# Performance work log

Measured on AMD Instinct MI355X. Metric: run time of the kernel, lower is better.

## Reference

```python
import jax, jax.numpy as jnp
import numpy as np

DIM = 256
NUM_HEADS = 8
HEAD_DIM = DIM // NUM_HEADS


def setup_inputs() -> dict:
    key = jax.random.key(0)
    k1, k2, k3, k4 = jax.random.split(key, 4)
    b, n = 4, 2048
    x = jax.random.normal(k1, (b, n, DIM), dtype=jnp.float32)
    # Linear weights with fan-in scaling (matches nn.Linear init magnitude,
    # keeps exp(qk) numerically sane since the original has no max-subtraction).
    Wqkv = jax.random.normal(k2, (DIM, 3 * DIM), dtype=jnp.float32) * (DIM ** -0.5)
    Wout = jax.random.normal(k3, (DIM, DIM), dtype=jnp.float32) * (DIM ** -0.5)
    bout = jax.random.normal(k4, (DIM,), dtype=jnp.float32) * 0.01
    return {"x": x, "Wqkv": Wqkv, "Wout": Wout, "bout": bout}


def reference(x, Wqkv, Wout, bout):
    b, n, d = x.shape
    h, hd = NUM_HEADS, HEAD_DIM
    scale = hd ** -0.5
    qkv = x @ Wqkv  # [b, n, 3d]
    q, k, v = jnp.split(qkv, 3, axis=-1)
    # [b, h, n, hd]
    q = q.reshape(b, n, h, hd).transpose(0, 2, 1, 3) * scale
    k = k.reshape(b, n, h, hd).transpose(0, 2, 1, 3)
    v = v.reshape(b, n, h, hd).transpose(0, 2, 1, 3)
    # Original KeOps path: unnormalized exp (no max-subtraction), separate
    # numerator / denominator reductions, eps in denominator.
    scores = jnp.einsum('bhnd,bhmd->bhnm', q, k)  # [b, h, n, n]
    e = jnp.exp(scores)
    denom = jnp.sum(e, axis=-1, keepdims=True)          # [b, h, n, 1]
    numer = jnp.einsum('bhnm,bhmd->bhnd', e, v)         # [b, h, n, hd]
    out = numer / (denom + 1e-6)
    out = out.transpose(0, 2, 1, 3).reshape(b, n, d)
    return out @ Wout + bout
```

## Files before the change

### kernel.cpp

```cpp
#include <hip/hip_runtime.h>

#define DIM 256
#define NHEADS 8
#define HDIM 32

typedef _Float16 half8_t __attribute__((ext_vector_type(8)));
typedef _Float16 half4_t __attribute__((ext_vector_type(4)));
typedef float float4_t __attribute__((ext_vector_type(4)));

__device__ __forceinline__ void gload_lds16(const void* g, void* l) {
    __builtin_amdgcn_global_load_lds((const __attribute__((address_space(1))) void*)g,
                                     (__attribute__((address_space(3))) void*)l,
                                     16, 0, 0);
}

#define QSCALE 0.25503093964976485f

__global__ __launch_bounds__(256) void prep_w(const float* __restrict__ Wqkv,
                                              const float* __restrict__ Wout,
                                              _Float16* __restrict__ WqT,
                                              _Float16* __restrict__ WoT) {
    __shared__ float ts[32][33];
    const int bid = blockIdx.x, t = threadIdx.x;
    const float* src; _Float16* dst; int N, kb, nb;
    if (bid < 192) { src = Wqkv; dst = WqT; N = 768; nb = bid % 24; kb = bid / 24; }
    else           { int b3 = bid - 192; src = Wout; dst = WoT; N = 256; nb = b3 % 8; kb = b3 / 8; }
    const int tx = t & 31, ty = t >> 5;
    #pragma unroll
    for (int i = 0; i < 4; ++i)
        ts[ty + i * 8][tx] = src[(size_t)(kb * 32 + ty + i * 8) * N + nb * 32 + tx];
    __syncthreads();
    #pragma unroll
    for (int i = 0; i < 4; ++i) {
        int nl = ty + i * 8;
        dst[(size_t)(nb * 32 + nl) * 256 + kb * 32 + tx] = (_Float16)ts[tx][nl];
    }
}

__global__ __launch_bounds__(256) void gemm_qkv(const float* __restrict__ x,
                                                const _Float16* __restrict__ BT,
                                                _Float16* __restrict__ qh,
                                                _Float16* __restrict__ kpack,
                                                _Float16* __restrict__ vp) {
    __shared__ alignas(16) _Float16 As[64 * 32];
    __shared__ alignas(16) _Float16 Bs[128 * 32];
    const int t = threadIdx.x, lane = t & 63, wave = t >> 6;
    const int l16 = lane & 15, quad = lane >> 4;
    const int m0 = blockIdx.y * 64, n0 = blockIdx.x * 128;
    const int wr = (wave >> 1) * 32, wc = (wave & 1) * 64;
    const int K = 256;

    float4_t acc[2][4];
    #pragma unroll
    for (int i = 0; i < 2; ++i)
        #pragma unroll
        for (int j = 0; j < 4; ++j) acc[i][j] = (float4_t){0.f, 0.f, 0.f, 0.f};

    const int arow = t >> 2;
    const int acol = (t & 3) * 8;
    const int srow = lane >> 2;
    const int scol = (lane & 3) * 8;

    for (int k0 = 0; k0 < K; k0 += 32) {
        {
            const float* xp = x + (size_t)(m0 + arow) * K + k0 + acol;
            float tmp[8];
            *reinterpret_cast<float4*>(tmp)     = *reinterpret_cast<const float4*>(xp);
            *reinterpret_cast<float4*>(tmp + 4) = *reinterpret_cast<const float4*>(xp + 4);
            half8_t h;
            #pragma unroll
            for (int j = 0; j < 8; ++j) h[j] = (_Float16)tmp[j];
            *reinterpret_cast<half8_t*>(As + arow * 32 + acol) = h;
        }
        gload_lds16(BT + (size_t)(n0 + wave * 16 + srow) * K + k0 + scol, Bs + wave * 512);
        gload_lds16(BT + (size_t)(n0 + 64 + wave * 16 + srow) * K + k0 + scol, Bs + 2048 + wave * 512);
        __syncthreads();
        half8_t af[2], bf[4];
        #pragma unroll
        for (int i = 0; i < 2; ++i)
            af[i] = *reinterpret_cast<const half8_t*>(As + (wr + i * 16 + l16) * 32 + quad * 8);
        #pragma unroll
        for (int j = 0; j < 4; ++j)
            bf[j] = *reinterpret_cast<const half8_t*>(Bs + (wc + j * 16 + l16) * 32 + quad * 8);
        #pragma unroll
        for (int i = 0; i < 2; ++i)
            #pragma unroll
            for (int j = 0; j < 4; ++j)
                acc[i][j] = __builtin_amdgcn_mfma_f32_16x16x32_f16(af[i], bf[j], acc[i][j], 0, 0, 0);
        __syncthreads();
    }

    const int bb = m0 >> 11;
    if (n0 < 256) {
        #pragma unroll
        for (int i = 0; i < 2; ++i)
            #pragma unroll
            for (int r = 0; r < 4; ++r) {
                int row = m0 + wr + i * 16 + quad * 4 + r;
                #pragma unroll
                for (int j = 0; j < 4; ++j)
                    qh[(size_t)row * 256 + n0 + wc + j * 16 + l16] =
                        (_Float16)(acc[i][j][r] * QSCALE);
            }
    } else if (n0 < 512) {
        #pragma unroll
        for (int i = 0; i < 2; ++i)
            #pragma unroll
            for (int r = 0; r < 4; ++r) {
                int tok = (m0 & 2047) + wr + i * 16 + quad * 4 + r;
                #pragma unroll
                for (int j = 0; j < 4; ++j) {
                    int kc = n0 + wc + j * 16 + l16 - 256;
                    int hh = kc >> 5, dd = kc & 31;
                    kpack[((size_t)(bb * NHEADS + hh) * 2048 + tok) * 32 + dd] =
                        (_Float16)acc[i][j][r];
                }
            }
    } else {
        #pragma unroll
        for (int i = 0; i < 2; ++i) {
            int tok0 = (m0 & 2047) + wr + i * 16 + quad * 4;
            int chunk = tok0 >> 5, tl = tok0 & 31;
            #pragma unroll
            for (int j = 0; j < 4; ++j) {
                int vc = n0 + wc + j * 16 + l16 - 512;
                int hh = vc >> 5, dd = vc & 31;
                half4_t p;
                #pragma unroll
                for (int r = 0; r < 4; ++r) p[r] = (_Float16)acc[i][j][r];
                *reinterpret_cast<half4_t*>(
                    vp + (((size_t)(bb * NHEADS + hh) * 64 + chunk) * 32 + dd) * 32 + tl) = p;
            }
        }
    }
}

__global__ __launch_bounds__(256, 2) void attn_v10(const _Float16* __restrict__ qh,
                                                   const _Float16* __restrict__ kpack,
                                                   const _Float16* __restrict__ vp,
                                                   _Float16* __restrict__ NUM,
                                                   float* __restrict__ DEN) {
    __shared__ alignas(16) _Float16 es[4][64][40];
    const int bid = blockIdx.x;
    const int kh = bid & 1;
    const int qb = (bid >> 1) & 7;
    const int bh = bid >> 4;
    const int b = bh >> 3, h = bh & 7;
    const int t = threadIdx.x, lane = t & 63, wave = t >> 6;
    const int l16 = lane & 15, quad = lane >> 4;
    const int bN = b * 2048;
    const int q0w = qb * 256 + wave * 64;
    const int kbeg = kh * 1024;

    half8_t qf[4];
    {
        const _Float16* qrow = qh + (size_t)(bN + q0w + l16) * 256 + h * HDIM + quad * 8;
        #pragma unroll
        for (int g = 0; g < 4; ++g)
            qf[g] = *reinterpret_cast<const half8_t*>(qrow + (size_t)g * 16 * 256);
    }

    const _Float16* kb_ = kpack + (size_t)bh * 65536;
    const _Float16* vb_ = vp + (size_t)bh * 65536;

    float4_t num[4][2], dacc[4];
    #pragma unroll
    for (int g = 0; g < 4; ++g) {
        num[g][0] = (float4_t){0.f, 0.f, 0.f, 0.f};
        num[g][1] = (float4_t){0.f, 0.f, 0.f, 0.f};
        dacc[g]   = (float4_t){0.f, 0.f, 0.f, 0.f};
    }
    half8_t ones;
    #pragma unroll
    for (int j = 0; j < 8; ++j) ones[j] = (_Float16)1.0f;

    _Float16* esw = &es[wave][0][0];
    const float4_t z = {0.f, 0.f, 0.f, 0.f};

    for (int k0 = kbeg; k0 < kbeg + 1024; k0 += 64) {
        half8_t kf[4], vf[4];
        #pragma unroll
        for (int j = 0; j < 4; ++j)
            kf[j] = *reinterpret_cast<const half8_t*>(
                kb_ + (size_t)(k0 + j * 16 + l16) * 32 + quad * 8);
        const int c0 = k0 >> 5;
        #pragma unroll
        for (int s = 0; s < 2; ++s)
            #pragma unroll
            for (int m = 0; m < 2; ++m)
                vf[s * 2 + m] = *reinterpret_cast<const half8_t*>(
                    vb_ + ((size_t)(c0 + s) * 32 + m * 16 + l16) * 32 + quad * 8);

        float4_t st[4][4];
        #pragma unroll
        for (int kb = 0; kb < 4; ++kb)
            #pragma unroll
            for (int g = 0; g < 4; ++g)
                st[kb][g] = __builtin_amdgcn_mfma_f32_16x16x32_f16(kf[kb], qf[g], z, 0, 0, 0);

        half4_t ep[4][4];
        #pragma unroll
        for (int kb = 0; kb < 4; ++kb)
            #pragma unroll
            for (int g = 0; g < 4; ++g)
                #pragma unroll
                for (int r = 0; r < 4; ++r)
                    ep[kb][g][r] = (_Float16)__builtin_exp2f(st[kb][g][r]);

        #pragma unroll
        for (int s = 0; s < 2; ++s) {
            #pragma unroll
            for (int tt = 0; tt < 2; ++tt)
                #pragma unroll
                for (int g = 0; g < 4; ++g)
                    *reinterpret_cast<half4_t*>(
                        esw + (g * 16 + l16) * 40 + tt * 16 + quad * 4) = ep[s * 2 + tt][g];

            #pragma unroll
            for (int g = 0; g < 4; ++g) {
                half8_t ef = *reinterpret_cast<const half8_t*>(
                    esw + (g * 16 + l16) * 40 + quad * 8);
                num[g][0] = __builtin_amdgcn_mfma_f32_16x16x32_f16(ef, vf[s * 2],     num[g][0], 0, 0, 0);
                num[g][1] = __builtin_amdgcn_mfma_f32_16x16x32_f16(ef, vf[s * 2 + 1], num[g][1], 0, 0, 0);
                dacc[g]   = __builtin_amdgcn_mfma_f32_16x16x32_f16(ef, ones,          dacc[g],   0, 0, 0);
            }
        }
    }

    _Float16* ob = NUM + (size_t)kh * 2097152 + ((size_t)bh * 2048 + q0w) * 32;
    #pragma unroll
    for (int g = 0; g < 4; ++g)
        #pragma unroll
        for (int r = 0; r < 4; ++r) {
            size_t ro = (size_t)(g * 16 + quad * 4 + r) * 32;
            ob[ro + l16]      = (_Float16)num[g][0][r];
            ob[ro + 16 + l16] = (_Float16)num[g][1][r];
        }
    if (l16 == 0) {
        #pragma unroll
        for (int g = 0; g < 4; ++g)
            #pragma unroll
            for (int r = 0; r < 4; ++r)
                DEN[kh * 65536 + bh * 2048 + q0w + g * 16 + quad * 4 + r] = dacc[g][r];
    }
}

__global__ __launch_bounds__(256) void gemm2c(const _Float16* __restrict__ NUM,
                                              const float* __restrict__ DEN,
                                              const _Float16* __restrict__ BT,
                                              const float* __restrict__ bias,
                                              float* __restrict__ out) {
    __shared__ alignas(16) _Float16 As[64 * 32];
    __shared__ alignas(16) _Float16 Bs[64 * 32];
    const int t = threadIdx.x, lane = t & 63, wave = t >> 6;
    const int l16 = lane & 15, quad = lane >> 4;
    const int m0 = blockIdx.y * 64, n0 = blockIdx.x * 64;
    const int wr = (wave >> 1) * 32, wc = (wave & 1) * 32;
    const int bb = m0 >> 11;

    const int arow = t >> 2;
    const int acol = (t & 3) * 8;
    const int tok = (m0 + arow) & 2047;
    _Float16 rcp8[8];
    #pragma unroll
    for (int hh = 0; hh < 8; ++hh) {
        int di = (bb * 8 + hh) * 2048 + tok;
        rcp8[hh] = (_Float16)(1.f / (DEN[di] + DEN[di + 65536] + 1e-6f));
    }

    float4_t acc[2][2];
    #pragma unroll
    for (int i = 0; i < 2; ++i)
        #pragma unroll
        for (int j = 0; j < 2; ++j) acc[i][j] = (float4_t){0.f, 0.f, 0.f, 0.f};

    for (int k0 = 0; k0 < 256; k0 += 32) {
        const int hh = k0 >> 5;
        const _Float16* np = NUM + (((size_t)(bb * 8 + hh) * 2048 + tok) * 32) + acol;
        half8_t s0 = *reinterpret_cast<const half8_t*>(np);
        half8_t s1 = *reinterpret_cast<const half8_t*>(np + 2097152);
        *reinterpret_cast<half8_t*>(As + arow * 32 + acol) = (s0 + s1) * rcp8[hh];
        gload_lds16(BT + (size_t)(n0 + arow) * 256 + k0 + acol, Bs + t * 8);
        __syncthreads();
        half8_t af[2], bf[2];
        #pragma unroll
        for (int i = 0; i < 2; ++i)
            af[i] = *reinterpret_cast<const half8_t*>(As + (wr + i * 16 + l16) * 32 + quad * 8);
        #pragma unroll
        for (int j = 0; j < 2; ++j)
            bf[j] = *reinterpret_cast<const half8_t*>(Bs + (wc + j * 16 + l16) * 32 + quad * 8);
        #pragma unroll
        for (int i = 0; i < 2; ++i)
            #pragma unroll
            for (int j = 0; j < 2; ++j)
                acc[i][j] = __builtin_amdgcn_mfma_f32_16x16x32_f16(af[i], bf[j], acc[i][j], 0, 0, 0);
        __syncthreads();
    }

    #pragma unroll
    for (int i = 0; i < 2; ++i)
        #pragma unroll
        for (int r = 0; r < 4; ++r) {
            int row = m0 + wr + i * 16 + quad * 4 + r;
            #pragma unroll
            for (int j = 0; j < 2; ++j) {
                int col = n0 + wc + j * 16 + l16;
                out[(size_t)row * 256 + col] = acc[i][j][r] + bias[col];
            }
        }
}

extern "C" void kernel_launch(void* const* d_in, const int* in_sizes, int n_in,
                              void* d_out, int out_size, void* d_ws, size_t ws_size,
                              hipStream_t stream) {
    const float* x    = (const float*)d_in[0];
    const float* Wqkv = (const float*)d_in[1];
    const float* Wout = (const float*)d_in[2];
    const float* bout = (const float*)d_in[3];
    float* out = (float*)d_out;
    const int M = 8192;

    _Float16* WqT   = (_Float16*)d_ws;
    _Float16* WoT   = WqT + 768 * 256;
    _Float16* qh    = WoT + 256 * 256;
    _Float16* kpack = qh + (size_t)M * DIM;
    _Float16* vp    = kpack + (size_t)32 * 2048 * 32;
    _Float16* NUM   = vp + (size_t)32 * 2048 * 32;
    float*    DEN   = (float*)(NUM + (size_t)2 * M * DIM);

    hipLaunchKernelGGL(prep_w, dim3(256), dim3(256), 0, stream, Wqkv, Wout, WqT, WoT);
    hipLaunchKernelGGL(gemm_qkv, dim3(6, 128), dim3(256), 0, stream, x, WqT, qh, kpack, vp);
    hipLaunchKernelGGL(attn_v10, dim3(512), dim3(256), 0, stream, qh, kpack, vp, NUM, DEN);
    hipLaunchKernelGGL(gemm2c, dim3(4, 128), dim3(256), 0, stream, NUM, DEN, WoT, bout, out);
}
```

Measured before the change: 143.5 us.

## Shrink GEMM tiles for more blocks and compute attention denominator with VALU sums

The QKV projection GEMM drops from 64x128 to 64x64 tiles, and the output GEMM from 64x64 to 64x32, which doubles the grid of each to improve CU occupancy. In the attention kernel, the per-row exp sum was an MFMA against a ones vector; it is now scalar float adds per lane followed by cross-quad shuffles. This frees MFMA issue slots and keeps the denominator in fp32 before rounding. The smaller tiles re-read the x and NUM activations more times, and the new per-element adds put more work on the VALU.

```diff
diff --git a/kernel.cpp b/kernel.cpp
--- a/kernel.cpp
+++ b/kernel.cpp
@@ -43,18 +43,18 @@
                                                 _Float16* __restrict__ kpack,
                                                 _Float16* __restrict__ vp) {
     __shared__ alignas(16) _Float16 As[64 * 32];
-    __shared__ alignas(16) _Float16 Bs[128 * 32];
+    __shared__ alignas(16) _Float16 Bs[64 * 32];
     const int t = threadIdx.x, lane = t & 63, wave = t >> 6;
     const int l16 = lane & 15, quad = lane >> 4;
-    const int m0 = blockIdx.y * 64, n0 = blockIdx.x * 128;
-    const int wr = (wave >> 1) * 32, wc = (wave & 1) * 64;
+    const int m0 = blockIdx.y * 64, n0 = blockIdx.x * 64;
+    const int wr = (wave >> 1) * 32, wc = (wave & 1) * 32;
     const int K = 256;
 
-    float4_t acc[2][4];
+    float4_t acc[2][2];
     #pragma unroll
     for (int i = 0; i < 2; ++i)
         #pragma unroll
-        for (int j = 0; j < 4; ++j) acc[i][j] = (float4_t){0.f, 0.f, 0.f, 0.f};
+        for (int j = 0; j < 2; ++j) acc[i][j] = (float4_t){0.f, 0.f, 0.f, 0.f};
 
     const int arow = t >> 2;
     const int acol = (t & 3) * 8;
@@ -73,19 +73,18 @@
             *reinterpret_cast<half8_t*>(As + arow * 32 + acol) = h;
         }
         gload_lds16(BT + (size_t)(n0 + wave * 16 + srow) * K + k0 + scol, Bs + wave * 512);
-        gload_lds16(BT + (size_t)(n0 + 64 + wave * 16 + srow) * K + k0 + scol, Bs + 2048 + wave * 512);
         __syncthreads();
-        half8_t af[2], bf[4];
+        half8_t af[2], bf[2];
         #pragma unroll
         for (int i = 0; i < 2; ++i)
             af[i] = *reinterpret_cast<const half8_t*>(As + (wr + i * 16 + l16) * 32 + quad * 8);
         #pragma unroll
-        for (int j = 0; j < 4; ++j)
+        for (int j = 0; j < 2; ++j)
             bf[j] = *reinterpret_cast<const half8_t*>(Bs + (wc + j * 16 + l16) * 32 + quad * 8);
         #pragma unroll
         for (int i = 0; i < 2; ++i)
             #pragma unroll
-            for (int j = 0; j < 4; ++j)
+            for (int j = 0; j < 2; ++j)
                 acc[i][j] = __builtin_amdgcn_mfma_f32_16x16x32_f16(af[i], bf[j], acc[i][j], 0, 0, 0);
         __syncthreads();
     }
@@ -98,7 +97,7 @@
             for (int r = 0; r < 4; ++r) {
                 int row = m0 + wr + i * 16 + quad * 4 + r;
                 #pragma unroll
-                for (int j = 0; j < 4; ++j)
+                for (int j = 0; j < 2; ++j)
                     qh[(size_t)row * 256 + n0 + wc + j * 16 + l16] =
                         (_Float16)(acc[i][j][r] * QSCALE);
             }
@@ -109,7 +108,7 @@
             for (int r = 0; r < 4; ++r) {
                 int tok = (m0 & 2047) + wr + i * 16 + quad * 4 + r;
                 #pragma unroll
-                for (int j = 0; j < 4; ++j) {
+                for (int j = 0; j < 2; ++j) {
                     int kc = n0 + wc + j * 16 + l16 - 256;
                     int hh = kc >> 5, dd = kc & 31;
                     kpack[((size_t)(bb * NHEADS + hh) * 2048 + tok) * 32 + dd] =
@@ -122,7 +121,7 @@
             int tok0 = (m0 & 2047) + wr + i * 16 + quad * 4;
             int chunk = tok0 >> 5, tl = tok0 & 31;
             #pragma unroll
-            for (int j = 0; j < 4; ++j) {
+            for (int j = 0; j < 2; ++j) {
                 int vc = n0 + wc + j * 16 + l16 - 512;
                 int hh = vc >> 5, dd = vc & 31;
                 half4_t p;
@@ -135,7 +134,7 @@
     }
 }
 
-__global__ __launch_bounds__(256, 2) void attn_v10(const _Float16* __restrict__ qh,
+__global__ __launch_bounds__(256, 2) void attn_v11(const _Float16* __restrict__ qh,
                                                    const _Float16* __restrict__ kpack,
                                                    const _Float16* __restrict__ vp,
                                                    _Float16* __restrict__ NUM,
@@ -145,7 +144,8 @@
     const int kh = bid & 1;
     const int qb = (bid >> 1) & 7;
     const int bh = bid >> 4;
-    const int b = bh >> 3, h = bh & 7;
+    const int b = bh >> 3;
+    const int h = bh & 7;
     const int t = threadIdx.x, lane = t & 63, wave = t >> 6;
     const int l16 = lane & 15, quad = lane >> 4;
     const int bN = b * 2048;
@@ -163,16 +163,13 @@
     const _Float16* kb_ = kpack + (size_t)bh * 65536;
     const _Float16* vb_ = vp + (size_t)bh * 65536;
 
-    float4_t num[4][2], dacc[4];
+    float4_t num[4][2];
     #pragma unroll
     for (int g = 0; g < 4; ++g) {
         num[g][0] = (float4_t){0.f, 0.f, 0.f, 0.f};
         num[g][1] = (float4_t){0.f, 0.f, 0.f, 0.f};
-        dacc[g]   = (float4_t){0.f, 0.f, 0.f, 0.f};
-    }
-    half8_t ones;
-    #pragma unroll
-    for (int j = 0; j < 8; ++j) ones[j] = (_Float16)1.0f;
+    }
+    float ds[4] = {0.f, 0.f, 0.f, 0.f};
 
     _Float16* esw = &es[wave][0][0];
     const float4_t z = {0.f, 0.f, 0.f, 0.f};
@@ -204,8 +201,11 @@
             #pragma unroll
             for (int g = 0; g < 4; ++g)
                 #pragma unroll
-                for (int r = 0; r < 4; ++r)
-                    ep[kb][g][r] = (_Float16)__builtin_exp2f(st[kb][g][r]);
+                for (int r = 0; r < 4; ++r) {
+                    float e = __builtin_exp2f(st[kb][g][r]);
+                    ds[g] += e;
+                    ep[kb][g][r] = (_Float16)e;
+                }
 
         #pragma unroll
         for (int s = 0; s < 2; ++s) {
@@ -222,9 +222,14 @@
                     esw + (g * 16 + l16) * 40 + quad * 8);
                 num[g][0] = __builtin_amdgcn_mfma_f32_16x16x32_f16(ef, vf[s * 2],     num[g][0], 0, 0, 0);
                 num[g][1] = __builtin_amdgcn_mfma_f32_16x16x32_f16(ef, vf[s * 2 + 1], num[g][1], 0, 0, 0);
-                dacc[g]   = __builtin_amdgcn_mfma_f32_16x16x32_f16(ef, ones,          dacc[g],   0, 0, 0);
             }
         }
+    }
+
+    #pragma unroll
+    for (int g = 0; g < 4; ++g) {
+        ds[g] += __shfl_xor(ds[g], 16, 64);
+        ds[g] += __shfl_xor(ds[g], 32, 64);
     }
 
     _Float16* ob = NUM + (size_t)kh * 2097152 + ((size_t)bh * 2048 + q0w) * 32;
@@ -236,12 +241,10 @@
             ob[ro + l16]      = (_Float16)num[g][0][r];
             ob[ro + 16 + l16] = (_Float16)num[g][1][r];
         }
-    if (l16 == 0) {
+    if (quad == 0) {
         #pragma unroll
         for (int g = 0; g < 4; ++g)
-            #pragma unroll
-            for (int r = 0; r < 4; ++r)
-                DEN[kh * 65536 + bh * 2048 + q0w + g * 16 + quad * 4 + r] = dacc[g][r];
+            DEN[kh * 65536 + bh * 2048 + q0w + g * 16 + l16] = ds[g];
     }
 }
 
@@ -251,15 +254,17 @@
                                               const float* __restrict__ bias,
                                               float* __restrict__ out) {
     __shared__ alignas(16) _Float16 As[64 * 32];
-    __shared__ alignas(16) _Float16 Bs[64 * 32];
+    __shared__ alignas(16) _Float16 Bs[32 * 32];
     const int t = threadIdx.x, lane = t & 63, wave = t >> 6;
     const int l16 = lane & 15, quad = lane >> 4;
-    const int m0 = blockIdx.y * 64, n0 = blockIdx.x * 64;
-    const int wr = (wave >> 1) * 32, wc = (wave & 1) * 32;
+    const int m0 = blockIdx.y * 64, n0 = blockIdx.x * 32;
+    const int wr = (wave >> 1) * 32, wc = (wave & 1) * 16;
     const int bb = m0 >> 11;
 
     const int arow = t >> 2;
     const int acol = (t & 3) * 8;
+    const int srow = lane >> 2;
+    const int scol = (lane & 3) * 8;
     const int tok = (m0 + arow) & 2047;
     _Float16 rcp8[8];
     #pragma unroll
@@ -268,11 +273,9 @@
         rcp8[hh] = (_Float16)(1.f / (DEN[di] + DEN[di + 65536] + 1e-6f));
     }
 
-    float4_t acc[2][2];
-    #pragma unroll
-    for (int i = 0; i < 2; ++i)
-        #pragma unroll
-        for (int j = 0; j < 2; ++j) acc[i][j] = (float4_t){0.f, 0.f, 0.f, 0.f};
+    float4_t acc[2];
+    acc[0] = (float4_t){0.f, 0.f, 0.f, 0.f};
+    acc[1] = (float4_t){0.f, 0.f, 0.f, 0.f};
 
     for (int k0 = 0; k0 < 256; k0 += 32) {
         const int hh = k0 >> 5;
@@ -280,20 +283,17 @@
         half8_t s0 = *reinterpret_cast<const half8_t*>(np);
         half8_t s1 = *reinterpret_cast<const half8_t*>(np + 2097152);
         *reinterpret_cast<half8_t*>(As + arow * 32 + acol) = (s0 + s1) * rcp8[hh];
-        gload_lds16(BT + (size_t)(n0 + arow) * 256 + k0 + acol, Bs + t * 8);
+        if (wave < 2)
+            gload_lds16(BT + (size_t)(n0 + wave * 16 + srow) * 256 + k0 + scol,
+                        Bs + wave * 512);
         __syncthreads();
-        half8_t af[2], bf[2];
+        half8_t af[2], bf;
         #pragma unroll
         for (int i = 0; i < 2; ++i)
             af[i] = *reinterpret_cast<const half8_t*>(As + (wr + i * 16 + l16) * 32 + quad * 8);
-        #pragma unroll
-        for (int j = 0; j < 2; ++j)
-            bf[j] = *reinterpret_cast<const half8_t*>(Bs + (wc + j * 16 + l16) * 32 + quad * 8);
-        #pragma unroll
-        for (int i = 0; i < 2; ++i)
-            #pragma unroll
-            for (int j = 0; j < 2; ++j)
-                acc[i][j] = __builtin_amdgcn_mfma_f32_16x16x32_f16(af[i], bf[j], acc[i][j], 0, 0, 0);
+        bf = *reinterpret_cast<const half8_t*>(Bs + (wc + l16) * 32 + quad * 8);
+        acc[0] = __builtin_amdgcn_mfma_f32_16x16x32_f16(af[0], bf, acc[0], 0, 0, 0);
+        acc[1] = __builtin_amdgcn_mfma_f32_16x16x32_f16(af[1], bf, acc[1], 0, 0, 0);
         __syncthreads();
     }
 
@@ -302,11 +302,8 @@
         #pragma unroll
         for (int r = 0; r < 4; ++r) {
             int row = m0 + wr + i * 16 + quad * 4 + r;
-            #pragma unroll
-            for (int j = 0; j < 2; ++j) {
-                int col = n0 + wc + j * 16 + l16;
-                out[(size_t)row * 256 + col] = acc[i][j][r] + bias[col];
-            }
+            int col = n0 + wc + l16;
+            out[(size_t)row * 256 + col] = acc[i][r] + bias[col];
         }
 }
 
@@ -329,7 +326,7 @@
     float*    DEN   = (float*)(NUM + (size_t)2 * M * DIM);
 
     hipLaunchKernelGGL(prep_w, dim3(256), dim3(256), 0, stream, Wqkv, Wout, WqT, WoT);
-    hipLaunchKernelGGL(gemm_qkv, dim3(6, 128), dim3(256), 0, stream, x, WqT, qh, kpack, vp);
-    hipLaunchKernelGGL(attn_v10, dim3(512), dim3(256), 0, stream, qh, kpack, vp, NUM, DEN);
-    hipLaunchKernelGGL(gemm2c, dim3(4, 128), dim3(256), 0, stream, NUM, DEN, WoT, bout, out);
-}
+    hipLaunchKernelGGL(gemm_qkv, dim3(12, 128), dim3(256), 0, stream, x, WqT, qh, kpack, vp);
+    hipLaunchKernelGGL(attn_v11, dim3(512), dim3(256), 0, stream, qh, kpack, vp, NUM, DEN);
+    hipLaunchKernelGGL(gemm2c, dim3(8, 128), dim3(256), 0, stream, NUM, DEN, WoT, bout, out);
+}
```

Measured after the change: 147.2 us. +2.6%, slower.
